# Kernel tuning notes

Hardware: AMD Instinct MI355X
Metric: run time of the kernel (lower is better)

The kernel has to match this reference:

```python
import jax, jax.numpy as jnp
import numpy as np
import math

DIM = 512
NUM_HEADS = 8
DIM_HEAD = DIM // NUM_HEADS


def normalized_coords(h, w):
    # (h*w, 2) with (x, y) in [0, 1]
    y = jnp.linspace(0.0, 1.0, h)
    x = jnp.linspace(0.0, 1.0, w)
    yg, xg = jnp.meshgrid(y, x, indexing='ij')
    return jnp.stack([xg.ravel(), yg.ravel()], axis=-1)


def rotate_half(x):
    dh = x.shape[-1] // 2
    return jnp.concatenate([-x[..., dh:], x[..., :dh]], axis=-1)


def apply_rope(t, coords):
    # t: (n, heads, seq, dim_head); coords: (seq, 2) (identical across batch)
    dim_half = t.shape[-1] // 2
    freq = 1.0 / (10000.0 ** (jnp.arange(dim_half, dtype=jnp.float32) / dim_half))
    ang_x = coords[:, 0:1] * freq  # (seq, dim_half)
    ang_y = coords[:, 1:2] * freq
    ang = jnp.concatenate([ang_x, ang_y], axis=-1)  # (seq, dim_head)
    cos, sin = jnp.cos(ang), jnp.sin(ang)
    return t * cos + rotate_half(t) * sin


def setup_inputs() -> dict:
    key = jax.random.key(0)
    ks = jax.random.split(key, 12)
    n, Np, d, H, W = 4, 1024, DIM, 64, 64
    s = 0.02
    return {
        'local_feat': jax.random.normal(ks[0], (n, Np, d), jnp.float32),
        'global_feat': jax.random.normal(ks[1], (n, d, H, W), jnp.float32),
        'Wq': jax.random.normal(ks[2], (d, d), jnp.float32) * s,
        'bq': jnp.zeros((d,), jnp.float32),
        'Wk': jax.random.normal(ks[3], (d, d), jnp.float32) * s,
        'bk': jnp.zeros((d,), jnp.float32),
        'Wv': jax.random.normal(ks[4], (d, d), jnp.float32) * s,
        'bv': jnp.zeros((d,), jnp.float32),
        'Wg': jax.random.normal(ks[5], (d, 2 * d), jnp.float32) * s,
        'bg': jnp.zeros((d,), jnp.float32),
        'Wo': jax.random.normal(ks[6], (d, d), jnp.float32) * s,
        'bo': jnp.zeros((d,), jnp.float32),
    }


def reference(local_feat, global_feat, Wq, bq, Wk, bk, Wv, bv, Wg, bg, Wo, bo):
    n, Np, d = local_feat.shape
    _, _, H, W = global_feat.shape
    h, dh = NUM_HEADS, DIM_HEAD
    gf = global_feat.reshape(n, d, H * W).transpose(0, 2, 1)  # (n, HW, d)

    P = int(math.isqrt(Np))
    local_coords = normalized_coords(P, P)      # (Np, 2)
    global_coords = normalized_coords(H, W)     # (HW, 2)

    def proj(x, Wt, b):
        return x @ Wt.T + b

    Q = proj(local_feat, Wq, bq).reshape(n, Np, h, dh).transpose(0, 2, 1, 3)
    K = proj(gf, Wk, bk).reshape(n, H * W, h, dh).transpose(0, 2, 1, 3)
    V = proj(gf, Wv, bv).reshape(n, H * W, h, dh).transpose(0, 2, 1, 3)

    Q = apply_rope(Q, local_coords)
    K = apply_rope(K, global_coords)

    scores = jnp.einsum('bhqd,bhkd->bhqk', Q, K) / math.sqrt(dh)
    attn = jax.nn.softmax(scores, axis=-1)
    ao = jnp.einsum('bhqk,bhkd->bhqd', attn, V)
    ao = ao.transpose(0, 2, 1, 3).reshape(n, Np, d)

    gate = jax.nn.sigmoid(jnp.concatenate([local_feat, ao], axis=-1) @ Wg.T + bg)
    enhanced = local_feat + gate * ao
    return enhanced @ Wo.T + bo
```

## Files before the change

kernel.cpp:

```cpp
#include <hip/hip_runtime.h>
#include <hip/hip_bf16.h>
#include <cstdint>

typedef __hip_bfloat16 BF;
typedef unsigned short ushort_t;
typedef __attribute__((ext_vector_type(8))) __bf16 bf16x8;
typedef __attribute__((ext_vector_type(4))) float f32x4;
typedef __attribute__((ext_vector_type(2))) unsigned uv2;
typedef __attribute__((ext_vector_type(4))) unsigned uint4v;

__device__ __forceinline__ float bu2f(ushort_t u) {
  return __uint_as_float((unsigned)u << 16);
}
__device__ __forceinline__ unsigned pk2(float a, float b) {
  union { __hip_bfloat162 h; unsigned u; } c;
  c.h = __float22bfloat162_rn(make_float2(a, b));
  return c.u;
}
__device__ __forceinline__ unsigned short f2bu(float f) {
  union { BF b; unsigned short u; } c; c.b = __float2bfloat16(f); return c.u;
}
__device__ __forceinline__ float b2f(BF x) { return __bfloat162float(x); }
__device__ __forceinline__ void rd16f(const float* fp, ushort_t* out) {
#pragma unroll
  for (int j = 0; j < 16; j += 4) {
    float4 v = *(const float4*)(fp + j);
    ((unsigned*)out)[j / 2] = pk2(v.x, v.y);
    ((unsigned*)out)[j / 2 + 1] = pk2(v.z, v.w);
  }
}

__device__ __forceinline__ void qswapB5(unsigned& a, unsigned& b) {
  uv2 r = __builtin_amdgcn_permlane32_swap(a, b, false, false);
  a = r[0]; b = r[1];
}
__device__ __forceinline__ void qswapB4(unsigned& a, unsigned& b, int lane) {
#if __has_builtin(__builtin_amdgcn_permlane16_swap)
  uv2 r = __builtin_amdgcn_permlane16_swap(a, b, false, false);
  a = r[0]; b = r[1];
#else
  unsigned as = __builtin_amdgcn_ds_swizzle(a, 0x401F);
  unsigned bs = __builtin_amdgcn_ds_swizzle(b, 0x401F);
  bool hi = (lane & 16) != 0;
  unsigned na = hi ? bs : a;
  unsigned nb = hi ? b : as;
  a = na; b = nb;
#endif
}

#define QS 0.1803368801111f

__global__ __launch_bounds__(256) void pre_k(const float* __restrict__ local,
                                             const float* __restrict__ gfeat,
                                             const float* __restrict__ Wq,
                                             const float* __restrict__ bq,
                                             BF* __restrict__ gfT,
                                             BF* __restrict__ Qb) {
  __shared__ __align__(16) ushort_t smem[2][64][72];
  const int t = threadIdx.x;
  if (blockIdx.x < 2048) {
    auto T = smem[0];
    const int g = blockIdx.x;
    const int bz = g & 3, mt = (g >> 2) & 63, kt = g >> 8;
    {
      int krow = t >> 2, mg = t & 3;
      ushort_t vals[16];
      rd16f(gfeat + (size_t)bz * 512 * 4096 + (size_t)(kt * 64 + krow) * 4096 +
                mt * 64 + mg * 16,
            vals);
#pragma unroll
      for (int j = 0; j < 16; ++j) T[mg * 16 + j][krow] = vals[j];
    }
    __syncthreads();
    int mrow = t >> 2, kg = t & 3;
    uint4 a = *(const uint4*)&T[mrow][kg * 16];
    uint4 b = *(const uint4*)&T[mrow][kg * 16 + 8];
    size_t o = ((size_t)bz * 4096 + mt * 64 + mrow) * 512 + kt * 64 + kg * 16;
    *(uint4*)&gfT[o] = a;
    *(uint4*)&gfT[o + 8] = b;
    return;
  }
  auto As = smem[0];
  auto Bs = smem[1];
  const int bx = blockIdx.x - 2048;
  const int m0 = (bx & 63) * 64, n0 = (bx >> 6) * 64;
  const int w = t >> 6, lane = t & 63;
  const int quad = lane >> 4, l16 = lane & 15;

  f32x4 acc[4] = {};
  for (int k0 = 0; k0 < 512; k0 += 64) {
    __syncthreads();
    {
      int row = t >> 2, cg = t & 3;
      int kg = k0 + cg * 16;
      ushort_t vals[16];
      rd16f(local + (size_t)(m0 + row) * 512 + kg, vals);
      *(uint4*)&As[row][cg * 16] = *(uint4*)&vals[0];
      *(uint4*)&As[row][cg * 16 + 8] = *(uint4*)&vals[8];
      ushort_t bv[16];
      rd16f(Wq + (size_t)(n0 + row) * 512 + kg, bv);
      *(uint4*)&Bs[row][cg * 16] = *(uint4*)&bv[0];
      *(uint4*)&Bs[row][cg * 16 + 8] = *(uint4*)&bv[8];
    }
    __syncthreads();
#pragma unroll
    for (int kc = 0; kc < 2; ++kc) {
      bf16x8 af = *(const bf16x8*)&As[w * 16 + l16][kc * 32 + quad * 8];
#pragma unroll
      for (int nt = 0; nt < 4; ++nt) {
        bf16x8 bfv = *(const bf16x8*)&Bs[nt * 16 + l16][kc * 32 + quad * 8];
        acc[nt] = __builtin_amdgcn_mfma_f32_16x16x32_bf16(af, bfv, acc[nt], 0, 0, 0);
      }
    }
  }
  const int head = n0 >> 6;
#pragma unroll
  for (int r = 0; r < 4; ++r) {
    int mg = m0 + w * 16 + quad * 4 + r;
    int bb = mg >> 10, qi = mg & 1023;
    float x = (float)(qi & 31) * (1.f / 31.f);
    float y = (float)(qi >> 5) * (1.f / 31.f);
    size_t base = (((size_t)bb * 8 + head) * 1024 + qi) * 64;
#pragma unroll
    for (int j = 0; j < 2; ++j) {
      int c0 = j * 16 + l16;
      float t0 = acc[j][r] + bq[head * 64 + c0];
      float t1 = acc[j + 2][r] + bq[head * 64 + c0 + 32];
      float fr = __expf((float)c0 * (-9.210340371976184f / 32.f));
      float ax = x * fr, ay = y * fr;
      Qb[base + c0] = __float2bfloat16((t0 * __cosf(ax) - t1 * __sinf(ax)) * QS);
      Qb[base + c0 + 32] = __float2bfloat16((t1 * __cosf(ay) + t0 * __sinf(ay)) * QS);
    }
  }
}

__global__ __launch_bounds__(256) void kv_k(const BF* __restrict__ gfT,
                                            const float* __restrict__ Wk,
                                            const float* __restrict__ Wv,
                                            const float* __restrict__ bk,
                                            const float* __restrict__ bv,
                                            BF* __restrict__ Kb,
                                            BF* __restrict__ VTb) {
  __shared__ __align__(16) ushort_t smem[2][128][72];
  auto As = smem[0];
  auto Bs = smem[1];
  const int tid = threadIdx.x;
  const int w = tid >> 6, lane = tid & 63;
  const int quad = lane >> 4, l16 = lane & 15;
  const int wm = w >> 1, wn = w & 1;
  const int g = blockIdx.x;
  const int a = g & 7, y = (g >> 3) & 7, bidx = g >> 6;
  const int m0 = ((bidx << 1) | (a & 1)) * 128;
  const int n0 = y * 128;
  const int bz = a >> 1;

  f32x4 acc[4][4] = {};
  for (int k0 = 0; k0 < 512; k0 += 64) {
    __syncthreads();
#pragma unroll
    for (int u = 0; u < 2; ++u) {
      int unit = tid + u * 256;
      int row = unit >> 2, cg = unit & 3;
      const uint4* p = (const uint4*)(gfT + ((size_t)bz * 4096 + m0 + row) * 512 +
                                      k0 + cg * 16);
      *(uint4*)&As[row][cg * 16] = p[0];
      *(uint4*)&As[row][cg * 16 + 8] = p[1];
    }
#pragma unroll
    for (int u = 0; u < 2; ++u) {
      int unit = tid + u * 256;
      int row = unit >> 2, cg = unit & 3;
      const float* bsrc = (n0 >= 512) ? Wv : Wk;
      size_t nrow = (n0 >= 512) ? (n0 - 512 + row) : (n0 + row);
      ushort_t vals[16];
      rd16f(bsrc + nrow * 512 + k0 + cg * 16, vals);
      *(uint4*)&Bs[row][cg * 16] = *(uint4*)&vals[0];
      *(uint4*)&Bs[row][cg * 16 + 8] = *(uint4*)&vals[8];
    }
    __syncthreads();
#pragma unroll
    for (int kc = 0; kc < 2; ++kc) {
      bf16x8 af[4], bfv[4];
#pragma unroll
      for (int i = 0; i < 4; ++i) {
        af[i] = *(const bf16x8*)&As[wm * 64 + i * 16 + l16][kc * 32 + quad * 8];
        bfv[i] = *(const bf16x8*)&Bs[wn * 64 + i * 16 + l16][kc * 32 + quad * 8];
      }
#pragma unroll
      for (int mt = 0; mt < 4; ++mt)
#pragma unroll
        for (int nt = 0; nt < 4; ++nt)
          acc[mt][nt] = __builtin_amdgcn_mfma_f32_16x16x32_bf16(af[mt], bfv[nt], acc[mt][nt], 0, 0, 0);
    }
  }
  if (n0 < 512) {
    const int head = (n0 + wn * 64) >> 6;
#pragma unroll
    for (int mt = 0; mt < 4; ++mt)
#pragma unroll
      for (int r = 0; r < 4; ++r) {
        int pg = m0 + wm * 64 + mt * 16 + quad * 4 + r;
        float x = (float)(pg & 63) * (1.f / 63.f);
        float yy = (float)(pg >> 6) * (1.f / 63.f);
        size_t base = (((size_t)bz * 8 + head) * 4096 + pg) * 64;
#pragma unroll
        for (int j = 0; j < 2; ++j) {
          int c0 = j * 16 + l16;
          float t0 = acc[mt][j][r] + bk[head * 64 + c0];
          float t1 = acc[mt][j + 2][r] + bk[head * 64 + c0 + 32];
          float fr = __expf((float)c0 * (-9.210340371976184f / 32.f));
          float ax = x * fr, ay = yy * fr;
          Kb[base + c0] = __float2bfloat16(t0 * __cosf(ax) - t1 * __sinf(ax));
          Kb[base + c0 + 32] = __float2bfloat16(t1 * __cosf(ay) + t0 * __sinf(ay));
        }
      }
  } else {
    const int n0v = n0 - 512;
    __syncthreads();
    ushort_t (*T)[136] = (ushort_t(*)[136]) & smem[0][0][0];
#pragma unroll
    for (int mt = 0; mt < 4; ++mt)
#pragma unroll
      for (int nt = 0; nt < 4; ++nt)
#pragma unroll
        for (int r = 0; r < 4; ++r) {
          int n_l = wn * 64 + nt * 16 + l16;
          int m_l = wm * 64 + mt * 16 + quad * 4 + r;
          T[n_l][m_l] = f2bu(acc[mt][nt][r] + bv[n0v + n_l]);
        }
    __syncthreads();
    int row = tid >> 1, half = tid & 1;
    size_t gbase = (((size_t)bz * 8 + (n0v >> 6) + (row >> 6)) * 64 + (row & 63)) * 4096 +
                   m0 + half * 64;
    uint4* dst = (uint4*)(VTb + gbase);
    const uint4* src = (const uint4*)&T[row][half * 64];
#pragma unroll
    for (int j = 0; j < 8; ++j) dst[j] = src[j];
  }
}

template <int NS>
__global__ __launch_bounds__(256, 4) void attn_k(const BF* __restrict__ Q,
                                                 const BF* __restrict__ K,
                                                 const BF* __restrict__ VT,
                                                 BF* __restrict__ AO,
                                                 BF* __restrict__ Opart,
                                                 float* __restrict__ lpart) {
  __shared__ __align__(16) ushort_t Ks[2][64][64];
  __shared__ __align__(16) ushort_t VTs[2][64][64];

  const int tid = threadIdx.x;
  const int w = tid >> 6, lane = tid & 63;
  const int quad = lane >> 4, l16 = lane & 15;
  const int r3 = l16 & 7;
  const int sc0 = (quad ^ r3) << 3;
  const int sc1 = sc0 ^ 32;

  const int g = blockIdx.x;
  const int bh = g & 31;
  const int qt = (g >> 5) & 7;
  const int ks = g >> 8;
  const int b = bh >> 3, h = bh & 7;
  const int q0 = qt * 128 + w * 32;
  const int kspan = 4096 / NS, kbase = ks * kspan;

  bf16x8 qa[2][2];
#pragma unroll
  for (int qs = 0; qs < 2; ++qs) {
    const BF* qp = Q + (((size_t)bh << 10) + q0 + qs * 16 + l16) * 64 + quad * 8;
    qa[qs][0] = *(const bf16x8*)qp;
    qa[qs][1] = *(const bf16x8*)(qp + 32);
  }
  bf16x8 ones;
#pragma unroll
  for (int j = 0; j < 8; ++j) ones[j] = (__bf16)1.0f;

  const BF* Kp = K + (size_t)bh * 4096 * 64;
  const BF* VTp = VT + (size_t)bh * 64 * 4096;

  f32x4 o[2][4] = {};
  f32x4 ol[2] = {};

  const int srow = tid >> 2, scol = (tid & 3) * 16;
  const int ssc = ((2 * (tid & 3)) ^ (srow & 7)) << 3;
  {
    const uint4* kp = (const uint4*)(Kp + (size_t)(kbase + srow) * 64 + scol);
    const uint4* vp = (const uint4*)(VTp + (size_t)srow * 4096 + kbase + scol);
    uint4 a = kp[0], bb = kp[1], c = vp[0], d = vp[1];
    *(uint4*)&Ks[0][srow][ssc] = a;  *(uint4*)&Ks[0][srow][ssc ^ 8] = bb;
    *(uint4*)&VTs[0][srow][ssc] = c; *(uint4*)&VTs[0][srow][ssc ^ 8] = d;
  }
  __syncthreads();

  const int nc = kspan / 64;
  for (int c = 0; c < nc; ++c) {
    const int cur = c & 1;
    uint4 nk0, nk1, nv0, nv1;
    const bool more = (c + 1 < nc);
    if (more) {
      const int c1 = kbase + (c + 1) * 64;
      const uint4* kp = (const uint4*)(Kp + (size_t)(c1 + srow) * 64 + scol);
      const uint4* vp = (const uint4*)(VTp + (size_t)srow * 4096 + c1 + scol);
      nk0 = kp[0]; nk1 = kp[1]; nv0 = vp[0]; nv1 = vp[1];
    }

#pragma unroll
    for (int qs = 0; qs < 2; ++qs) {
      unsigned Sp[4][2];
#pragma unroll
      for (int ct = 0; ct < 4; ++ct) {
        const int krow = ct * 16 + l16;
        bf16x8 kb0 = *(const bf16x8*)&Ks[cur][krow][sc0];
        bf16x8 kb1 = *(const bf16x8*)&Ks[cur][krow][sc1];
        f32x4 s = {};
        __builtin_amdgcn_s_setprio(1);
        s = __builtin_amdgcn_mfma_f32_16x16x32_bf16(kb0, qa[qs][0], s, 0, 0, 0);
        s = __builtin_amdgcn_mfma_f32_16x16x32_bf16(kb1, qa[qs][1], s, 0, 0, 0);
        __builtin_amdgcn_s_setprio(0);
        Sp[ct][0] = pk2(__builtin_exp2f(s[0]), __builtin_exp2f(s[1]));
        Sp[ct][1] = pk2(__builtin_exp2f(s[2]), __builtin_exp2f(s[3]));
      }
      unsigned pr[8];
#pragma unroll
      for (int hf = 0; hf < 2; ++hf) {
#pragma unroll
        for (int hh = 0; hh < 2; ++hh) {
          unsigned aa = Sp[hf * 2][hh], bb2 = Sp[hf * 2 + 1][hh];
          qswapB5(aa, bb2);
          qswapB4(aa, bb2, lane);
          pr[hf * 4 + hh] = aa;
          pr[hf * 4 + 2 + hh] = bb2;
        }
      }
      uint4v u0 = {pr[0], pr[1], pr[2], pr[3]};
      uint4v u1 = {pr[4], pr[5], pr[6], pr[7]};
      bf16x8 pa0 = __builtin_bit_cast(bf16x8, u0);
      bf16x8 pa1 = __builtin_bit_cast(bf16x8, u1);

      __builtin_amdgcn_s_setprio(1);
      ol[qs] = __builtin_amdgcn_mfma_f32_16x16x32_bf16(ones, pa0, ol[qs], 0, 0, 0);
      ol[qs] = __builtin_amdgcn_mfma_f32_16x16x32_bf16(ones, pa1, ol[qs], 0, 0, 0);
#pragma unroll
      for (int nt = 0; nt < 4; ++nt) {
        const int vrow = nt * 16 + l16;
        bf16x8 vb0 = *(const bf16x8*)&VTs[cur][vrow][sc0];
        bf16x8 vb1 = *(const bf16x8*)&VTs[cur][vrow][sc1];
        o[qs][nt] = __builtin_amdgcn_mfma_f32_16x16x32_bf16(vb0, pa0, o[qs][nt], 0, 0, 0);
        o[qs][nt] = __builtin_amdgcn_mfma_f32_16x16x32_bf16(vb1, pa1, o[qs][nt], 0, 0, 0);
      }
      __builtin_amdgcn_s_setprio(0);
    }

    if (more) {
      *(uint4*)&Ks[cur ^ 1][srow][ssc] = nk0;
      *(uint4*)&Ks[cur ^ 1][srow][ssc ^ 8] = nk1;
      *(uint4*)&VTs[cur ^ 1][srow][ssc] = nv0;
      *(uint4*)&VTs[cur ^ 1][srow][ssc ^ 8] = nv1;
    }
    __syncthreads();
  }

#pragma unroll
  for (int qs = 0; qs < 2; ++qs) {
    int qg = q0 + qs * 16 + l16;
    if (NS == 1) {
      float invl = 1.f / ol[qs][0];
#pragma unroll
      for (int nt = 0; nt < 4; ++nt) {
        uint2 uu;
        uu.x = pk2(o[qs][nt][0] * invl, o[qs][nt][1] * invl);
        uu.y = pk2(o[qs][nt][2] * invl, o[qs][nt][3] * invl);
        *(uint2*)(AO + (((size_t)b << 10) + qg) * 512 + h * 64 + nt * 16 + quad * 4) = uu;
      }
    } else {
      if (quad == 0) lpart[ks * 32768 + (bh << 10) + qg] = ol[qs][0];
#pragma unroll
      for (int nt = 0; nt < 4; ++nt) {
        uint2 uu;
        uu.x = pk2(o[qs][nt][0], o[qs][nt][1]);
        uu.y = pk2(o[qs][nt][2], o[qs][nt][3]);
        *(uint2*)(Opart + (size_t)ks * 2097152 + (((size_t)bh << 10) + qg) * 64 +
                  nt * 16 + quad * 4) = uu;
      }
    }
  }
}

template <int NS>
__global__ __launch_bounds__(256) void gate_k(const float* __restrict__ local,
                                              const BF* __restrict__ AO,
                                              const BF* __restrict__ Opart,
                                              const float* __restrict__ lpart,
                                              const float* __restrict__ Wg,
                                              const float* __restrict__ bg,
                                              BF* __restrict__ ENH) {
  __shared__ __align__(16) ushort_t As[64][72];
  __shared__ __align__(16) ushort_t Bs[64][72];
  const int tid = threadIdx.x;
  const int w = tid >> 6, lane = tid & 63;
  const int quad = lane >> 4, l16 = lane & 15;
  const int m0 = blockIdx.x * 64, n0 = blockIdx.y * 64;

  f32x4 acc[4] = {};
  float aosv[4][4];
  for (int k0 = 0; k0 < 1024; k0 += 64) {
    __syncthreads();
    {
      int row = tid >> 2, cg = tid & 3;
      int kg = k0 + cg * 16;
      ushort_t vals[16];
      if (kg < 512) {
        rd16f(local + (size_t)(m0 + row) * 512 + kg, vals);
      } else {
        int c = kg - 512;
        int hh = c >> 6, dh0 = c & 63;
        int mg = m0 + row;
        size_t bq = (size_t)(((mg >> 10) * 8 + hh) << 10) + (mg & 1023);
        if (NS == 1) {
          const uint4* p = (const uint4*)(AO + (size_t)mg * 512 + c);
          *(uint4*)&vals[0] = p[0]; *(uint4*)&vals[8] = p[1];
        } else {
          float ls = 0.f;
#pragma unroll
          for (int s2 = 0; s2 < NS; ++s2) ls += lpart[s2 * 32768 + bq];
          float inv = 1.f / ls;
          float av[16] = {};
#pragma unroll
          for (int s2 = 0; s2 < NS; ++s2) {
            const ushort_t* op = (const ushort_t*)Opart + (size_t)s2 * 2097152 +
                                 bq * 64 + dh0;
            uint4 u0 = ((const uint4*)op)[0], u1 = ((const uint4*)op)[1];
            const ushort_t* pu = (const ushort_t*)&u0;
#pragma unroll
            for (int j = 0; j < 8; ++j) av[j] += bu2f(pu[j]);
            pu = (const ushort_t*)&u1;
#pragma unroll
            for (int j = 0; j < 8; ++j) av[8 + j] += bu2f(pu[j]);
          }
#pragma unroll
          for (int j = 0; j < 16; j += 2)
            ((unsigned*)vals)[j / 2] = pk2(av[j] * inv, av[j + 1] * inv);
        }
      }
      *(uint4*)&As[row][cg * 16] = *(uint4*)&vals[0];
      *(uint4*)&As[row][cg * 16 + 8] = *(uint4*)&vals[8];
      ushort_t bv[16];
      rd16f(Wg + (size_t)(n0 + row) * 1024 + kg, bv);
      *(uint4*)&Bs[row][cg * 16] = *(uint4*)&bv[0];
      *(uint4*)&Bs[row][cg * 16 + 8] = *(uint4*)&bv[8];
    }
    __syncthreads();
    if (k0 == 512 + n0) {
#pragma unroll
      for (int r = 0; r < 4; ++r)
#pragma unroll
        for (int nt = 0; nt < 4; ++nt)
          aosv[r][nt] = bu2f(As[w * 16 + quad * 4 + r][nt * 16 + l16]);
    }
#pragma unroll
    for (int kc = 0; kc < 2; ++kc) {
      bf16x8 af = *(const bf16x8*)&As[w * 16 + l16][kc * 32 + quad * 8];
#pragma unroll
      for (int nt = 0; nt < 4; ++nt) {
        bf16x8 bfv = *(const bf16x8*)&Bs[nt * 16 + l16][kc * 32 + quad * 8];
        acc[nt] = __builtin_amdgcn_mfma_f32_16x16x32_bf16(af, bfv, acc[nt], 0, 0, 0);
      }
    }
  }
#pragma unroll
  for (int r = 0; r < 4; ++r) {
    int mg = m0 + w * 16 + quad * 4 + r;
#pragma unroll
    for (int nt = 0; nt < 4; ++nt) {
      int ng = n0 + nt * 16 + l16;
      size_t idx = (size_t)mg * 512 + ng;
      float gg = 1.f / (1.f + __expf(-(acc[nt][r] + bg[ng])));
      ENH[idx] = __float2bfloat16(local[idx] + gg * aosv[r][nt]);
    }
  }
}

__global__ __launch_bounds__(256) void out_k(const BF* __restrict__ ENH,
                                             const float* __restrict__ Wo,
                                             const float* __restrict__ bo,
                                             float* __restrict__ out) {
  __shared__ __align__(16) ushort_t As[64][72];
  __shared__ __align__(16) ushort_t Bs[64][72];
  const int tid = threadIdx.x;
  const int w = tid >> 6, lane = tid & 63;
  const int quad = lane >> 4, l16 = lane & 15;
  const int m0 = blockIdx.x * 64, n0 = blockIdx.y * 64;

  f32x4 acc[4] = {};
  for (int k0 = 0; k0 < 512; k0 += 64) {
    __syncthreads();
    {
      int row = tid >> 2, cg = tid & 3;
      int kg = k0 + cg * 16;
      const uint4* p = (const uint4*)(ENH + (size_t)(m0 + row) * 512 + kg);
      *(uint4*)&As[row][cg * 16] = p[0];
      *(uint4*)&As[row][cg * 16 + 8] = p[1];
      ushort_t bv[16];
      rd16f(Wo + (size_t)(n0 + row) * 512 + kg, bv);
      *(uint4*)&Bs[row][cg * 16] = *(uint4*)&bv[0];
      *(uint4*)&Bs[row][cg * 16 + 8] = *(uint4*)&bv[8];
    }
    __syncthreads();
#pragma unroll
    for (int kc = 0; kc < 2; ++kc) {
      bf16x8 af = *(const bf16x8*)&As[w * 16 + l16][kc * 32 + quad * 8];
#pragma unroll
      for (int nt = 0; nt < 4; ++nt) {
        bf16x8 bfv = *(const bf16x8*)&Bs[nt * 16 + l16][kc * 32 + quad * 8];
        acc[nt] = __builtin_amdgcn_mfma_f32_16x16x32_bf16(af, bfv, acc[nt], 0, 0, 0);
      }
    }
  }
#pragma unroll
  for (int r = 0; r < 4; ++r) {
    int mg = m0 + w * 16 + quad * 4 + r;
#pragma unroll
    for (int nt = 0; nt < 4; ++nt) {
      int ng = n0 + nt * 16 + l16;
      out[(size_t)mg * 512 + ng] = acc[nt][r] + bo[ng];
    }
  }
}

extern "C" void kernel_launch(void* const* d_in, const int* in_sizes, int n_in,
                              void* d_out, int out_size, void* d_ws, size_t ws_size,
                              hipStream_t stream) {
  const float* local = (const float*)d_in[0];
  const float* gfeat = (const float*)d_in[1];
  const float* Wq = (const float*)d_in[2];
  const float* bq = (const float*)d_in[3];
  const float* Wk = (const float*)d_in[4];
  const float* bk = (const float*)d_in[5];
  const float* Wv = (const float*)d_in[6];
  const float* bv = (const float*)d_in[7];
  const float* Wg = (const float*)d_in[8];
  const float* bg = (const float*)d_in[9];
  const float* Wo = (const float*)d_in[10];
  const float* bo = (const float*)d_in[11];

  char* w = (char*)d_ws;
  BF* Qb = (BF*)w;            w += (size_t)2097152 * 2;
  BF* Kb = (BF*)w;            w += (size_t)8388608 * 2;
  BF* VTb = (BF*)w;           w += (size_t)8388608 * 2;
  BF* AO = (BF*)w;            w += (size_t)2097152 * 2;
  BF* gfT = (BF*)w;
  BF* Opart = (BF*)w;
  size_t baseOff = (size_t)(w - (char*)d_ws);
  BF* ENH = Qb;

  int NS = 1;
  if (baseOff + 4 * (4194304 + 131072) <= ws_size) NS = 4;
  else if (baseOff + 16777216 + 2 * 131072 <= ws_size) NS = 2;
  float* lpart = (float*)(w + (size_t)NS * 4194304);

  dim3 blk(256);
  pre_k<<<dim3(2560), blk, 0, stream>>>(local, gfeat, Wq, bq, gfT, Qb);
  kv_k<<<dim3(1024), blk, 0, stream>>>(gfT, Wk, Wv, bk, bv, Kb, VTb);
  if (NS == 4) {
    attn_k<4><<<dim3(1024), blk, 0, stream>>>(Qb, Kb, VTb, AO, Opart, lpart);
    gate_k<4><<<dim3(64, 8), blk, 0, stream>>>(local, AO, Opart, lpart, Wg, bg, ENH);
  } else if (NS == 2) {
    attn_k<2><<<dim3(512), blk, 0, stream>>>(Qb, Kb, VTb, AO, Opart, lpart);
    gate_k<2><<<dim3(64, 8), blk, 0, stream>>>(local, AO, Opart, lpart, Wg, bg, ENH);
  } else {
    attn_k<1><<<dim3(256), blk, 0, stream>>>(Qb, Kb, VTb, AO, nullptr, nullptr);
    gate_k<1><<<dim3(64, 8), blk, 0, stream>>>(local, AO, Opart, lpart, Wg, bg, ENH);
  }
  out_k<<<dim3(64, 8), blk, 0, stream>>>(ENH, Wo, bo, (float*)d_out);
}
```

Measured before the change: 249.5 us.

## Permute V shared-memory layout to drop lane-permute shuffles in attention

Stores the transposed V tile into shared memory with a column permutation that matches the MFMA output layout of the score tile. The exponentiated scores can then feed the PV MFMA directly, which removes the permlane32/permlane16 swap shuffles. The loops are also reordered so each K and V fragment read from LDS is reused across both query sub-tiles. In exchange, V is staged with four 8-byte LDS stores instead of two 16-byte stores, which may raise bank conflicts or store count.

```diff
diff --git a/kernel.cpp b/kernel.cpp
--- a/kernel.cpp
+++ b/kernel.cpp
@@ -6,7 +6,6 @@
 typedef unsigned short ushort_t;
 typedef __attribute__((ext_vector_type(8))) __bf16 bf16x8;
 typedef __attribute__((ext_vector_type(4))) float f32x4;
-typedef __attribute__((ext_vector_type(2))) unsigned uv2;
 typedef __attribute__((ext_vector_type(4))) unsigned uint4v;
 
 __device__ __forceinline__ float bu2f(ushort_t u) {
@@ -28,24 +27,6 @@
     ((unsigned*)out)[j / 2] = pk2(v.x, v.y);
     ((unsigned*)out)[j / 2 + 1] = pk2(v.z, v.w);
   }
-}
-
-__device__ __forceinline__ void qswapB5(unsigned& a, unsigned& b) {
-  uv2 r = __builtin_amdgcn_permlane32_swap(a, b, false, false);
-  a = r[0]; b = r[1];
-}
-__device__ __forceinline__ void qswapB4(unsigned& a, unsigned& b, int lane) {
-#if __has_builtin(__builtin_amdgcn_permlane16_swap)
-  uv2 r = __builtin_amdgcn_permlane16_swap(a, b, false, false);
-  a = r[0]; b = r[1];
-#else
-  unsigned as = __builtin_amdgcn_ds_swizzle(a, 0x401F);
-  unsigned bs = __builtin_amdgcn_ds_swizzle(b, 0x401F);
-  bool hi = (lane & 16) != 0;
-  unsigned na = hi ? bs : a;
-  unsigned nb = hi ? b : as;
-  a = na; b = nb;
-#endif
 }
 
 #define QS 0.1803368801111f
@@ -283,12 +264,29 @@
 
   const int srow = tid >> 2, scol = (tid & 3) * 16;
   const int ssc = ((2 * (tid & 3)) ^ (srow & 7)) << 3;
+  int vcol[4];
+  {
+    const int s1 = (tid >> 1) & 1, s0v = tid & 1;
+#pragma unroll
+    for (int gq = 0; gq < 4; ++gq)
+      vcol[gq] = (((s1 * 4 + gq) ^ (srow & 7)) << 3) + s0v * 4;
+  }
+
+#define STAGE_V(buf, v0, v1)                                   \
+  {                                                            \
+    uint2 t_;                                                  \
+    t_.x = (v0).x; t_.y = (v0).y; *(uint2*)&VTs[buf][srow][vcol[0]] = t_; \
+    t_.x = (v0).z; t_.y = (v0).w; *(uint2*)&VTs[buf][srow][vcol[1]] = t_; \
+    t_.x = (v1).x; t_.y = (v1).y; *(uint2*)&VTs[buf][srow][vcol[2]] = t_; \
+    t_.x = (v1).z; t_.y = (v1).w; *(uint2*)&VTs[buf][srow][vcol[3]] = t_; \
+  }
+
   {
     const uint4* kp = (const uint4*)(Kp + (size_t)(kbase + srow) * 64 + scol);
     const uint4* vp = (const uint4*)(VTp + (size_t)srow * 4096 + kbase + scol);
     uint4 a = kp[0], bb = kp[1], c = vp[0], d = vp[1];
     *(uint4*)&Ks[0][srow][ssc] = a;  *(uint4*)&Ks[0][srow][ssc ^ 8] = bb;
-    *(uint4*)&VTs[0][srow][ssc] = c; *(uint4*)&VTs[0][srow][ssc ^ 8] = d;
+    STAGE_V(0, c, d);
   }
   __syncthreads();
 
@@ -304,61 +302,62 @@
       nk0 = kp[0]; nk1 = kp[1]; nv0 = vp[0]; nv1 = vp[1];
     }
 
-#pragma unroll
-    for (int qs = 0; qs < 2; ++qs) {
-      unsigned Sp[4][2];
-#pragma unroll
-      for (int ct = 0; ct < 4; ++ct) {
-        const int krow = ct * 16 + l16;
-        bf16x8 kb0 = *(const bf16x8*)&Ks[cur][krow][sc0];
-        bf16x8 kb1 = *(const bf16x8*)&Ks[cur][krow][sc1];
+    unsigned pa_u[2][2][4];
+#pragma unroll
+    for (int ct = 0; ct < 4; ++ct) {
+      const int krow = ct * 16 + l16;
+      bf16x8 kb0 = *(const bf16x8*)&Ks[cur][krow][sc0];
+      bf16x8 kb1 = *(const bf16x8*)&Ks[cur][krow][sc1];
+#pragma unroll
+      for (int qs = 0; qs < 2; ++qs) {
         f32x4 s = {};
         __builtin_amdgcn_s_setprio(1);
         s = __builtin_amdgcn_mfma_f32_16x16x32_bf16(kb0, qa[qs][0], s, 0, 0, 0);
         s = __builtin_amdgcn_mfma_f32_16x16x32_bf16(kb1, qa[qs][1], s, 0, 0, 0);
         __builtin_amdgcn_s_setprio(0);
-        Sp[ct][0] = pk2(__builtin_exp2f(s[0]), __builtin_exp2f(s[1]));
-        Sp[ct][1] = pk2(__builtin_exp2f(s[2]), __builtin_exp2f(s[3]));
-      }
-      unsigned pr[8];
-#pragma unroll
-      for (int hf = 0; hf < 2; ++hf) {
-#pragma unroll
-        for (int hh = 0; hh < 2; ++hh) {
-          unsigned aa = Sp[hf * 2][hh], bb2 = Sp[hf * 2 + 1][hh];
-          qswapB5(aa, bb2);
-          qswapB4(aa, bb2, lane);
-          pr[hf * 4 + hh] = aa;
-          pr[hf * 4 + 2 + hh] = bb2;
-        }
-      }
-      uint4v u0 = {pr[0], pr[1], pr[2], pr[3]};
-      uint4v u1 = {pr[4], pr[5], pr[6], pr[7]};
-      bf16x8 pa0 = __builtin_bit_cast(bf16x8, u0);
-      bf16x8 pa1 = __builtin_bit_cast(bf16x8, u1);
-
-      __builtin_amdgcn_s_setprio(1);
-      ol[qs] = __builtin_amdgcn_mfma_f32_16x16x32_bf16(ones, pa0, ol[qs], 0, 0, 0);
-      ol[qs] = __builtin_amdgcn_mfma_f32_16x16x32_bf16(ones, pa1, ol[qs], 0, 0, 0);
-#pragma unroll
-      for (int nt = 0; nt < 4; ++nt) {
-        const int vrow = nt * 16 + l16;
-        bf16x8 vb0 = *(const bf16x8*)&VTs[cur][vrow][sc0];
-        bf16x8 vb1 = *(const bf16x8*)&VTs[cur][vrow][sc1];
-        o[qs][nt] = __builtin_amdgcn_mfma_f32_16x16x32_bf16(vb0, pa0, o[qs][nt], 0, 0, 0);
-        o[qs][nt] = __builtin_amdgcn_mfma_f32_16x16x32_bf16(vb1, pa1, o[qs][nt], 0, 0, 0);
-      }
-      __builtin_amdgcn_s_setprio(0);
-    }
+        pa_u[qs][ct >> 1][(ct & 1) * 2] =
+            pk2(__builtin_exp2f(s[0]), __builtin_exp2f(s[1]));
+        pa_u[qs][ct >> 1][(ct & 1) * 2 + 1] =
+            pk2(__builtin_exp2f(s[2]), __builtin_exp2f(s[3]));
+      }
+    }
+    bf16x8 pa[2][2];
+#pragma unroll
+    for (int qs = 0; qs < 2; ++qs)
+#pragma unroll
+      for (int kk = 0; kk < 2; ++kk) {
+        uint4v u = {pa_u[qs][kk][0], pa_u[qs][kk][1], pa_u[qs][kk][2],
+                    pa_u[qs][kk][3]};
+        pa[qs][kk] = __builtin_bit_cast(bf16x8, u);
+      }
+
+    __builtin_amdgcn_s_setprio(1);
+#pragma unroll
+    for (int qs = 0; qs < 2; ++qs) {
+      ol[qs] = __builtin_amdgcn_mfma_f32_16x16x32_bf16(ones, pa[qs][0], ol[qs], 0, 0, 0);
+      ol[qs] = __builtin_amdgcn_mfma_f32_16x16x32_bf16(ones, pa[qs][1], ol[qs], 0, 0, 0);
+    }
+#pragma unroll
+    for (int nt = 0; nt < 4; ++nt) {
+      const int vrow = nt * 16 + l16;
+      bf16x8 vb0 = *(const bf16x8*)&VTs[cur][vrow][sc0];
+      bf16x8 vb1 = *(const bf16x8*)&VTs[cur][vrow][sc1];
+#pragma unroll
+      for (int qs = 0; qs < 2; ++qs) {
+        o[qs][nt] = __builtin_amdgcn_mfma_f32_16x16x32_bf16(vb0, pa[qs][0], o[qs][nt], 0, 0, 0);
+        o[qs][nt] = __builtin_amdgcn_mfma_f32_16x16x32_bf16(vb1, pa[qs][1], o[qs][nt], 0, 0, 0);
+      }
+    }
+    __builtin_amdgcn_s_setprio(0);
 
     if (more) {
       *(uint4*)&Ks[cur ^ 1][srow][ssc] = nk0;
       *(uint4*)&Ks[cur ^ 1][srow][ssc ^ 8] = nk1;
-      *(uint4*)&VTs[cur ^ 1][srow][ssc] = nv0;
-      *(uint4*)&VTs[cur ^ 1][srow][ssc ^ 8] = nv1;
-    }
-    __syncthreads();
-  }
+      STAGE_V(cur ^ 1, nv0, nv1);
+    }
+    __syncthreads();
+  }
+#undef STAGE_V
 
 #pragma unroll
   for (int qs = 0; qs < 2; ++qs) {
```

Result: no change. 248.2 us (-0.6%).
